# Performance work log

Hardware: AMD Instinct MI355X
Metric: run time of the kernel (lower is better)

## Reference

```python
import jax, jax.numpy as jnp
import numpy as np

E = 1024   # embed_dim
H = 16     # num_heads
HD = E // H
FF = 4096  # hidden_dim
EPS = 1e-5

def _ln(x, g, b):
    mu = jnp.mean(x, axis=-1, keepdims=True)
    var = jnp.mean((x - mu) ** 2, axis=-1, keepdims=True)
    return (x - mu) * jax.lax.rsqrt(var + EPS) * g + b

def setup_inputs() -> dict:
    key = jax.random.key(0)
    ks = jax.random.split(key, 8)
    s = 0.02
    return {
        "x": jax.random.normal(ks[0], (2, 2048, E), dtype=jnp.float32),
        "w_qkv": jax.random.normal(ks[1], (3 * E, E), dtype=jnp.float32) * s,
        "b_qkv": jnp.zeros((3 * E,), dtype=jnp.float32),
        "w_out": jax.random.normal(ks[2], (E, E), dtype=jnp.float32) * s,
        "b_out": jnp.zeros((E,), dtype=jnp.float32),
        "g1": jnp.ones((E,), dtype=jnp.float32),
        "beta1": jnp.zeros((E,), dtype=jnp.float32),
        "g2": jnp.ones((E,), dtype=jnp.float32),
        "beta2": jnp.zeros((E,), dtype=jnp.float32),
        "w1": jax.random.normal(ks[3], (FF, E), dtype=jnp.float32) * s,
        "bf1": jnp.zeros((FF,), dtype=jnp.float32),
        "w2": jax.random.normal(ks[4], (E, FF), dtype=jnp.float32) * s,
        "bf2": jnp.zeros((E,), dtype=jnp.float32),
    }

def reference(x, w_qkv, b_qkv, w_out, b_out, g1, beta1, g2, beta2, w1, bf1, w2, bf2):
    B, S, _ = x.shape
    # qkv projection, then the module's exact reshape: (B,S,H,3*HD) -> (H,B,S,3*HD)
    qkv = (x @ w_qkv.T + b_qkv).reshape(B, S, H, 3 * HD).transpose(2, 0, 1, 3)
    q, k, v = jnp.split(qkv, 3, axis=-1)           # each (H,B,S,HD)
    scores = jnp.einsum('hbqd,hbkd->hbqk', q, k) / (HD ** 0.5)
    attn = jax.nn.softmax(scores, axis=-1)
    ctx = jnp.einsum('hbqk,hbkd->hbqd', attn, v)   # (H,B,S,HD)
    ctx = ctx.transpose(1, 2, 0, 3).reshape(B, S, E)
    attn_out = ctx @ w_out.T + b_out
    x1 = _ln(x + attn_out, g1, beta1)
    # FFN with exact (erf-based) GELU, matching torch nn.GELU default
    h = jax.nn.gelu(x1 @ w1.T + bf1, approximate=False)
    ffn_out = h @ w2.T + bf2
    return _ln(x1 + ffn_out, g2, beta2)
```

## Files before the change

### kernel.cpp

```cpp
#include <hip/hip_runtime.h>
#include <hip/hip_bf16.h>
#include <math.h>

typedef __bf16 bf16x8 __attribute__((ext_vector_type(8)));
typedef __bf16 bf16x4 __attribute__((ext_vector_type(4)));
typedef float  f32x4  __attribute__((ext_vector_type(4)));

#define MFMA16(a, b, c) __builtin_amdgcn_mfma_f32_16x16x32_bf16((a), (b), (c), 0, 0, 0)

__device__ __forceinline__ void gl16(const void* g, void* l) {
  __builtin_amdgcn_global_load_lds(
      (const __attribute__((address_space(1))) unsigned int*)g,
      (__attribute__((address_space(3))) unsigned int*)l, 16, 0, 0);
}

__global__ __launch_bounds__(256) void f32_to_bf16(const float* __restrict__ in,
                                                   __bf16* __restrict__ out, int n) {
  int i = (blockIdx.x * 256 + threadIdx.x) * 4;
  if (i < n) {
    float4 f = *(const float4*)(in + i);
    bf16x4 o = {(__bf16)f.x, (__bf16)f.y, (__bf16)f.z, (__bf16)f.w};
    *(bf16x4*)(out + i) = o;
  }
}

template <int MODE>
__global__ __launch_bounds__(256, 2) void gemm_bt(
    const __bf16* __restrict__ A, const __bf16* __restrict__ Bw,
    const float* __restrict__ bias, const float* __restrict__ resid,
    float* __restrict__ outF, __bf16* __restrict__ outB, int M, int N, int K) {
  __shared__ __bf16 As[128 * 32];
  __shared__ __bf16 Bs[128 * 32];
  const int tid = threadIdx.x;
  const int wave = tid >> 6, lane = tid & 63;
  const int quad = lane >> 4, l16 = lane & 15;
  const int wm = (wave >> 1) * 64, wn = (wave & 1) * 64;
  const long bm = (long)blockIdx.y * 128, bn = (long)blockIdx.x * 128;
  const int r0 = tid >> 2;
  const int c0 = (tid & 3) * 8;
  const __bf16* Ag = A + (bm + r0) * (long)K + c0;
  const __bf16* Bg = Bw + (bn + r0) * (long)K + c0;

  f32x4 acc[4][4] = {};

  for (int k0 = 0; k0 < K; k0 += 32) {
    __syncthreads();
    gl16(Ag + k0, &As[tid * 8]);
    gl16(Ag + 64 * (long)K + k0, &As[2048 + tid * 8]);
    gl16(Bg + k0, &Bs[tid * 8]);
    gl16(Bg + 64 * (long)K + k0, &Bs[2048 + tid * 8]);
    __syncthreads();

    bf16x8 af[4], bfr[4];
#pragma unroll
    for (int mt = 0; mt < 4; mt++)
      af[mt] = *(const bf16x8*)&As[(wm + mt * 16 + l16) * 32 + quad * 8];
#pragma unroll
    for (int nt = 0; nt < 4; nt++)
      bfr[nt] = *(const bf16x8*)&Bs[(wn + nt * 16 + l16) * 32 + quad * 8];
#pragma unroll
    for (int nt = 0; nt < 4; nt++)
#pragma unroll
      for (int mt = 0; mt < 4; mt++)
        acc[mt][nt] = MFMA16(af[mt], bfr[nt], acc[mt][nt]);
  }

#pragma unroll
  for (int mt = 0; mt < 4; mt++) {
#pragma unroll
    for (int nt = 0; nt < 4; nt++) {
#pragma unroll
      for (int r = 0; r < 4; r++) {
        const int row = (int)bm + wm + mt * 16 + quad * 4 + r;
        const int col = (int)bn + wn + nt * 16 + l16;
        float v = acc[mt][nt][r] + bias[col];
        if (MODE == 0) {
          const int b = row >> 11, s = row & 2047;
          const int h = col / 192, rem = col - h * 192;
          const int seg = rem >> 6, d = rem & 63;
          const int hb = h * 2 + b;
          if (seg == 0) {
            v *= 0.180336880111113704f;
            outB[((long)hb * 2048 + s) * 64 + d] = (__bf16)v;
          } else if (seg == 1) {
            outB[4194304L + ((long)hb * 2048 + s) * 64 + d] = (__bf16)v;
          } else {
            const int t = s >> 6, kp = s & 63;
            outB[2 * 4194304L + (((long)hb * 32 + t) * 64 + d) * 64 + kp] = (__bf16)v;
          }
        } else if (MODE == 2) {
          const float g = 0.5f * v * (1.0f + erff(v * 0.70710678118654752f));
          outB[(long)row * N + col] = (__bf16)g;
        } else {
          const long idx = (long)row * N + col;
          outF[idx] = resid[idx] + v;
        }
      }
    }
  }
}

__global__ __launch_bounds__(256, 2) void gemm_bt64(
    const __bf16* __restrict__ A, const __bf16* __restrict__ Bw,
    const float* __restrict__ bias, const float* __restrict__ resid,
    float* __restrict__ outF, int M, int N, int K) {
  __shared__ __bf16 As[64 * 32];
  __shared__ __bf16 Bs[128 * 32];
  const int tid = threadIdx.x;
  const int wave = tid >> 6, lane = tid & 63;
  const int quad = lane >> 4, l16 = lane & 15;
  const int wm = (wave >> 1) * 32, wn = (wave & 1) * 64;
  const long bm = (long)blockIdx.y * 64, bn = (long)blockIdx.x * 128;
  const int r0 = tid >> 2;
  const int c0 = (tid & 3) * 8;
  const __bf16* Ag = A + (bm + r0) * (long)K + c0;
  const __bf16* Bg = Bw + (bn + r0) * (long)K + c0;

  f32x4 acc[2][4] = {};

  for (int k0 = 0; k0 < K; k0 += 32) {
    __syncthreads();
    gl16(Ag + k0, &As[tid * 8]);
    gl16(Bg + k0, &Bs[tid * 8]);
    gl16(Bg + 64 * (long)K + k0, &Bs[2048 + tid * 8]);
    __syncthreads();

    bf16x8 af[2], bfr[4];
#pragma unroll
    for (int mt = 0; mt < 2; mt++)
      af[mt] = *(const bf16x8*)&As[(wm + mt * 16 + l16) * 32 + quad * 8];
#pragma unroll
    for (int nt = 0; nt < 4; nt++)
      bfr[nt] = *(const bf16x8*)&Bs[(wn + nt * 16 + l16) * 32 + quad * 8];
#pragma unroll
    for (int nt = 0; nt < 4; nt++)
#pragma unroll
      for (int mt = 0; mt < 2; mt++)
        acc[mt][nt] = MFMA16(af[mt], bfr[nt], acc[mt][nt]);
  }

#pragma unroll
  for (int mt = 0; mt < 2; mt++)
#pragma unroll
    for (int nt = 0; nt < 4; nt++)
#pragma unroll
      for (int r = 0; r < 4; r++) {
        const int row = (int)bm + wm + mt * 16 + quad * 4 + r;
        const int col = (int)bn + wn + nt * 16 + l16;
        const float v = acc[mt][nt][r] + bias[col];
        const long idx = (long)row * N + col;
        outF[idx] = resid[idx] + v;
      }
}

__global__ __launch_bounds__(256) void flash_attn(const __bf16* __restrict__ Qb,
                                                  const __bf16* __restrict__ Kb,
                                                  const __bf16* __restrict__ Vtb,
                                                  __bf16* __restrict__ ctx) {
  __shared__ __bf16 KsLo[64 * 32], KsHi[64 * 32];
  __shared__ __bf16 VsLo[64 * 32], VsHi[64 * 32];
  __shared__ __bf16 Pb[4][32 * 72];
  const int tid = threadIdx.x;
  const int wave = tid >> 6, lane = tid & 63;
  const int quad = lane >> 4, l16 = lane & 15;
  const int n = blockIdx.x;
  const int hb = n & 31;
  const int qblk = n >> 5;
  const int h = hb >> 1, b = hb & 1;
  const __bf16* Q = Qb + (long)hb * 131072;
  const __bf16* K = Kb + (long)hb * 131072;
  const __bf16* Vt = Vtb + (long)hb * 131072;
  const int qr = qblk * 128 + wave * 32;

  bf16x8 q0[2], q1[2];
#pragma unroll
  for (int rb = 0; rb < 2; rb++) {
    q0[rb] = *(const bf16x8*)&Q[(qr + rb * 16 + l16) * 64 + quad * 8];
    q1[rb] = *(const bf16x8*)&Q[(qr + rb * 16 + l16) * 64 + 32 + quad * 8];
  }

  f32x4 o[2][4] = {};
  f32x4 lp[2] = {};

  const int sr = tid >> 2;
  const int sc = (tid & 3) * 8;

  for (int kt = 0; kt < 2048; kt += 64) {
    __syncthreads();
    gl16(&K[(kt + sr) * 64 + sc], &KsLo[tid * 8]);
    gl16(&K[(kt + sr) * 64 + 32 + sc], &KsHi[tid * 8]);
    const __bf16* Vtile = Vt + (long)(kt >> 6) * 4096;
    gl16(&Vtile[sr * 64 + sc], &VsLo[tid * 8]);
    gl16(&Vtile[sr * 64 + 32 + sc], &VsHi[tid * 8]);
    __syncthreads();

    bf16x8 kf0[4], kf1[4];
#pragma unroll
    for (int nt = 0; nt < 4; nt++) {
      kf0[nt] = *(const bf16x8*)&KsLo[(nt * 16 + l16) * 32 + quad * 8];
      kf1[nt] = *(const bf16x8*)&KsHi[(nt * 16 + l16) * 32 + quad * 8];
    }
    f32x4 s[2][4];
#pragma unroll
    for (int rb = 0; rb < 2; rb++)
#pragma unroll
      for (int nt = 0; nt < 4; nt++) {
        f32x4 z = {};
        z = MFMA16(q0[rb], kf0[nt], z);
        z = MFMA16(q1[rb], kf1[nt], z);
        s[rb][nt] = z;
      }

#pragma unroll
    for (int rb = 0; rb < 2; rb++)
#pragma unroll
      for (int nt = 0; nt < 4; nt++)
#pragma unroll
        for (int r = 0; r < 4; r++) {
          const float p = __builtin_amdgcn_exp2f(s[rb][nt][r]);
          s[rb][nt][r] = p;
          lp[rb][r] += p;
        }

#pragma unroll
    for (int rb = 0; rb < 2; rb++)
#pragma unroll
      for (int nt = 0; nt < 4; nt++)
#pragma unroll
        for (int r = 0; r < 4; r++)
          Pb[wave][(rb * 16 + quad * 4 + r) * 72 + nt * 16 + l16] =
              (__bf16)s[rb][nt][r];

    bf16x8 vf0[4], vf1[4];
#pragma unroll
    for (int nt = 0; nt < 4; nt++) {
      vf0[nt] = *(const bf16x8*)&VsLo[(nt * 16 + l16) * 32 + quad * 8];
      vf1[nt] = *(const bf16x8*)&VsHi[(nt * 16 + l16) * 32 + quad * 8];
    }
#pragma unroll
    for (int rb = 0; rb < 2; rb++) {
      const bf16x8 p0 = *(const bf16x8*)&Pb[wave][(rb * 16 + l16) * 72 + quad * 8];
      const bf16x8 p1 = *(const bf16x8*)&Pb[wave][(rb * 16 + l16) * 72 + 32 + quad * 8];
#pragma unroll
      for (int nt = 0; nt < 4; nt++) {
        o[rb][nt] = MFMA16(p0, vf0[nt], o[rb][nt]);
        o[rb][nt] = MFMA16(p1, vf1[nt], o[rb][nt]);
      }
    }
  }

#pragma unroll
  for (int rb = 0; rb < 2; rb++) {
    float inv[4];
#pragma unroll
    for (int r = 0; r < 4; r++) {
      float l = lp[rb][r];
      l += __shfl_xor(l, 1);
      l += __shfl_xor(l, 2);
      l += __shfl_xor(l, 4);
      l += __shfl_xor(l, 8);
      inv[r] = __builtin_amdgcn_rcpf(l);
    }
#pragma unroll
    for (int nt = 0; nt < 4; nt++)
#pragma unroll
      for (int r = 0; r < 4; r++) {
        const int srow = qr + rb * 16 + quad * 4 + r;
        const float val = o[rb][nt][r] * inv[r];
        const int d = nt * 16 + l16;
        ctx[((long)(b * 2048 + srow)) * 1024 + h * 64 + d] = (__bf16)val;
      }
  }
}

template <int WB>
__global__ __launch_bounds__(256) void layernorm_k(const float* __restrict__ in,
                                                   const float* __restrict__ g,
                                                   const float* __restrict__ be,
                                                   float* __restrict__ outF,
                                                   __bf16* __restrict__ outB) {
  const int tid = threadIdx.x;
  const long row = blockIdx.x;
  const float4 v = ((const float4*)(in + row * 1024))[tid];
  float sum = v.x + v.y + v.z + v.w;
  float sq = v.x * v.x + v.y * v.y + v.z * v.z + v.w * v.w;
#pragma unroll
  for (int m = 32; m >= 1; m >>= 1) {
    sum += __shfl_xor(sum, m);
    sq += __shfl_xor(sq, m);
  }
  __shared__ float red[8];
  const int wave = tid >> 6;
  if ((tid & 63) == 0) {
    red[wave] = sum;
    red[4 + wave] = sq;
  }
  __syncthreads();
  sum = red[0] + red[1] + red[2] + red[3];
  sq = red[4] + red[5] + red[6] + red[7];
  const float mu = sum * (1.f / 1024.f);
  const float var = sq * (1.f / 1024.f) - mu * mu;
  const float rs = rsqrtf(var + 1e-5f);
  const float4 gv = ((const float4*)g)[tid];
  const float4 bv = ((const float4*)be)[tid];
  float4 o;
  o.x = (v.x - mu) * rs * gv.x + bv.x;
  o.y = (v.y - mu) * rs * gv.y + bv.y;
  o.z = (v.z - mu) * rs * gv.z + bv.z;
  o.w = (v.w - mu) * rs * gv.w + bv.w;
  ((float4*)(outF + row * 1024))[tid] = o;
  if (WB) {
    bf16x4 ob = {(__bf16)o.x, (__bf16)o.y, (__bf16)o.z, (__bf16)o.w};
    *(bf16x4*)&outB[row * 1024 + tid * 4] = ob;
  }
}

extern "C" void kernel_launch(void* const* d_in, const int* in_sizes, int n_in,
                              void* d_out, int out_size, void* d_ws, size_t ws_size,
                              hipStream_t stream) {
  const float* x     = (const float*)d_in[0];
  const float* w_qkv = (const float*)d_in[1];
  const float* b_qkv = (const float*)d_in[2];
  const float* w_out = (const float*)d_in[3];
  const float* b_out = (const float*)d_in[4];
  const float* g1    = (const float*)d_in[5];
  const float* be1   = (const float*)d_in[6];
  const float* g2    = (const float*)d_in[7];
  const float* be2   = (const float*)d_in[8];
  const float* w1    = (const float*)d_in[9];
  const float* bf1   = (const float*)d_in[10];
  const float* w2    = (const float*)d_in[11];
  const float* bf2   = (const float*)d_in[12];
  float* out = (float*)d_out;

  char* ws = (char*)d_ws;
  const long MB = 1024L * 1024;
  __bf16* wqkvb = (__bf16*)(ws + 0 * MB);
  __bf16* woutb = (__bf16*)(ws + 6 * MB);
  __bf16* w1b   = (__bf16*)(ws + 8 * MB);
  __bf16* w2b   = (__bf16*)(ws + 16 * MB);
  __bf16* xb    = (__bf16*)(ws + 24 * MB);
  __bf16* qkvb  = (__bf16*)(ws + 32 * MB);
  __bf16* ctxb  = (__bf16*)(ws + 56 * MB);
  float*  res1  = (float*)(ws + 64 * MB);
  __bf16* x1b   = (__bf16*)(ws + 80 * MB);
  __bf16* hb    = (__bf16*)(ws + 32 * MB);
  float*  res2  = (float*)(ws + 0 * MB);

  f32_to_bf16<<<4096, 256, 0, stream>>>(x, xb, 4096 * 1024);
  f32_to_bf16<<<3072, 256, 0, stream>>>(w_qkv, wqkvb, 3072 * 1024);
  f32_to_bf16<<<1024, 256, 0, stream>>>(w_out, woutb, 1024 * 1024);
  f32_to_bf16<<<4096, 256, 0, stream>>>(w1, w1b, 4096 * 1024);
  f32_to_bf16<<<4096, 256, 0, stream>>>(w2, w2b, 1024 * 4096);

  gemm_bt<0><<<dim3(24, 32), 256, 0, stream>>>(xb, wqkvb, b_qkv, nullptr, nullptr,
                                               qkvb, 4096, 3072, 1024);
  flash_attn<<<512, 256, 0, stream>>>(qkvb, qkvb + 4194304,
                                      qkvb + 2 * 4194304, ctxb);
  gemm_bt64<<<dim3(8, 64), 256, 0, stream>>>(ctxb, woutb, b_out, x, res1,
                                             4096, 1024, 1024);
  layernorm_k<1><<<4096, 256, 0, stream>>>(res1, g1, be1, res1, x1b);
  gemm_bt<2><<<dim3(32, 32), 256, 0, stream>>>(x1b, w1b, bf1, nullptr, nullptr, hb,
                                               4096, 4096, 1024);
  gemm_bt64<<<dim3(8, 64), 256, 0, stream>>>(hb, w2b, bf2, res1, res2,
                                             4096, 1024, 4096);
  layernorm_k<0><<<4096, 256, 0, stream>>>(res2, g2, be2, out, nullptr);
}
```

Baseline: 398.2 us.

## Split-K the N=1024 GEMMs and fuse partial reduction into LayerNorm

Replaces the 64-row output-projection and FFN-down GEMMs with a 128x128-tile split-K kernel (4 K-slices). Each slice writes bf16 partial sums into workspace regions that are no longer live. A new reduce_ln kernel sums the partials, adds bias and residual, and applies LayerNorm in one pass. This removes the separate fp32 residual round-trip and gives more parallel blocks for the long-K GEMM. The five weight and input cast launches are also merged into one kernel. Storing partials in bf16 adds extra rounding error, and the scheme depends on carefully aliased workspace buffers.

```diff
diff --git a/kernel.cpp b/kernel.cpp
--- a/kernel.cpp
+++ b/kernel.cpp
@@ -14,21 +14,31 @@
       (__attribute__((address_space(3))) unsigned int*)l, 16, 0, 0);
 }
 
-__global__ __launch_bounds__(256) void f32_to_bf16(const float* __restrict__ in,
-                                                   __bf16* __restrict__ out, int n) {
-  int i = (blockIdx.x * 256 + threadIdx.x) * 4;
-  if (i < n) {
-    float4 f = *(const float4*)(in + i);
-    bf16x4 o = {(__bf16)f.x, (__bf16)f.y, (__bf16)f.z, (__bf16)f.w};
-    *(bf16x4*)(out + i) = o;
-  }
+__global__ __launch_bounds__(256) void cast_all(
+    const float* __restrict__ x, const float* __restrict__ wqkv,
+    const float* __restrict__ wout, const float* __restrict__ w1,
+    const float* __restrict__ w2, __bf16* __restrict__ xb,
+    __bf16* __restrict__ wqkvb, __bf16* __restrict__ woutb,
+    __bf16* __restrict__ w1b, __bf16* __restrict__ w2b) {
+  const long i = ((long)blockIdx.x * 256 + threadIdx.x) * 4;
+  const float* src;
+  __bf16* dst;
+  long off;
+  if (i < 4194304L) { src = x; dst = xb; off = i; }
+  else if (i < 7340032L) { src = wqkv; dst = wqkvb; off = i - 4194304L; }
+  else if (i < 8388608L) { src = wout; dst = woutb; off = i - 7340032L; }
+  else if (i < 12582912L) { src = w1; dst = w1b; off = i - 8388608L; }
+  else { src = w2; dst = w2b; off = i - 12582912L; }
+  const float4 f = *(const float4*)(src + off);
+  bf16x4 o = {(__bf16)f.x, (__bf16)f.y, (__bf16)f.z, (__bf16)f.w};
+  *(bf16x4*)(dst + off) = o;
 }
 
 template <int MODE>
 __global__ __launch_bounds__(256, 2) void gemm_bt(
     const __bf16* __restrict__ A, const __bf16* __restrict__ Bw,
-    const float* __restrict__ bias, const float* __restrict__ resid,
-    float* __restrict__ outF, __bf16* __restrict__ outB, int M, int N, int K) {
+    const float* __restrict__ bias, __bf16* __restrict__ outB,
+    int M, int N, int K) {
   __shared__ __bf16 As[128 * 32];
   __shared__ __bf16 Bs[128 * 32];
   const int tid = threadIdx.x;
@@ -88,46 +98,45 @@
             const int t = s >> 6, kp = s & 63;
             outB[2 * 4194304L + (((long)hb * 32 + t) * 64 + d) * 64 + kp] = (__bf16)v;
           }
-        } else if (MODE == 2) {
+        } else {
           const float g = 0.5f * v * (1.0f + erff(v * 0.70710678118654752f));
           outB[(long)row * N + col] = (__bf16)g;
-        } else {
-          const long idx = (long)row * N + col;
-          outF[idx] = resid[idx] + v;
         }
       }
     }
   }
 }
 
-__global__ __launch_bounds__(256, 2) void gemm_bt64(
+__global__ __launch_bounds__(256, 2) void gemm_split(
     const __bf16* __restrict__ A, const __bf16* __restrict__ Bw,
-    const float* __restrict__ bias, const float* __restrict__ resid,
-    float* __restrict__ outF, int M, int N, int K) {
-  __shared__ __bf16 As[64 * 32];
+    __bf16* __restrict__ Pbase, const long4 offs, int N, int K, int splitK) {
+  __shared__ __bf16 As[128 * 32];
   __shared__ __bf16 Bs[128 * 32];
   const int tid = threadIdx.x;
   const int wave = tid >> 6, lane = tid & 63;
   const int quad = lane >> 4, l16 = lane & 15;
-  const int wm = (wave >> 1) * 32, wn = (wave & 1) * 64;
-  const long bm = (long)blockIdx.y * 64, bn = (long)blockIdx.x * 128;
+  const int wm = (wave >> 1) * 64, wn = (wave & 1) * 64;
+  const long bm = (long)blockIdx.y * 128, bn = (long)blockIdx.x * 128;
+  const int z = blockIdx.z;
+  const long kb = (long)z * splitK;
   const int r0 = tid >> 2;
   const int c0 = (tid & 3) * 8;
-  const __bf16* Ag = A + (bm + r0) * (long)K + c0;
-  const __bf16* Bg = Bw + (bn + r0) * (long)K + c0;
-
-  f32x4 acc[2][4] = {};
-
-  for (int k0 = 0; k0 < K; k0 += 32) {
+  const __bf16* Ag = A + (bm + r0) * (long)K + c0 + kb;
+  const __bf16* Bg = Bw + (bn + r0) * (long)K + c0 + kb;
+
+  f32x4 acc[4][4] = {};
+
+  for (int k0 = 0; k0 < splitK; k0 += 32) {
     __syncthreads();
     gl16(Ag + k0, &As[tid * 8]);
+    gl16(Ag + 64 * (long)K + k0, &As[2048 + tid * 8]);
     gl16(Bg + k0, &Bs[tid * 8]);
     gl16(Bg + 64 * (long)K + k0, &Bs[2048 + tid * 8]);
     __syncthreads();
 
-    bf16x8 af[2], bfr[4];
-#pragma unroll
-    for (int mt = 0; mt < 2; mt++)
+    bf16x8 af[4], bfr[4];
+#pragma unroll
+    for (int mt = 0; mt < 4; mt++)
       af[mt] = *(const bf16x8*)&As[(wm + mt * 16 + l16) * 32 + quad * 8];
 #pragma unroll
     for (int nt = 0; nt < 4; nt++)
@@ -135,22 +144,72 @@
 #pragma unroll
     for (int nt = 0; nt < 4; nt++)
 #pragma unroll
-      for (int mt = 0; mt < 2; mt++)
+      for (int mt = 0; mt < 4; mt++)
         acc[mt][nt] = MFMA16(af[mt], bfr[nt], acc[mt][nt]);
   }
 
-#pragma unroll
-  for (int mt = 0; mt < 2; mt++)
+  const long po = (z == 0) ? offs.x : (z == 1) ? offs.y : (z == 2) ? offs.z : offs.w;
+#pragma unroll
+  for (int mt = 0; mt < 4; mt++)
 #pragma unroll
     for (int nt = 0; nt < 4; nt++)
 #pragma unroll
       for (int r = 0; r < 4; r++) {
         const int row = (int)bm + wm + mt * 16 + quad * 4 + r;
         const int col = (int)bn + wn + nt * 16 + l16;
-        const float v = acc[mt][nt][r] + bias[col];
-        const long idx = (long)row * N + col;
-        outF[idx] = resid[idx] + v;
-      }
+        Pbase[po + (long)row * N + col] = (__bf16)acc[mt][nt][r];
+      }
+}
+
+template <int WB>
+__global__ __launch_bounds__(256) void reduce_ln(
+    const __bf16* __restrict__ Pbase, const long4 offs,
+    const float* __restrict__ resid, const float* __restrict__ bias,
+    const float* __restrict__ g, const float* __restrict__ be,
+    float* __restrict__ outF, __bf16* __restrict__ outB) {
+  const int tid = threadIdx.x;
+  const long row = blockIdx.x;
+  const int c = tid * 4;
+  float4 v = ((const float4*)(resid + row * 1024))[tid];
+  const float4 bb = ((const float4*)bias)[tid];
+  v.x += bb.x; v.y += bb.y; v.z += bb.z; v.w += bb.w;
+  const long lo[4] = {offs.x, offs.y, offs.z, offs.w};
+#pragma unroll
+  for (int s = 0; s < 4; s++) {
+    const bf16x4 p = *(const bf16x4*)&Pbase[lo[s] + row * 1024 + c];
+    v.x += (float)p[0]; v.y += (float)p[1]; v.z += (float)p[2]; v.w += (float)p[3];
+  }
+  float sum = v.x + v.y + v.z + v.w;
+  float sq = v.x * v.x + v.y * v.y + v.z * v.z + v.w * v.w;
+#pragma unroll
+  for (int m = 32; m >= 1; m >>= 1) {
+    sum += __shfl_xor(sum, m);
+    sq += __shfl_xor(sq, m);
+  }
+  __shared__ float red[8];
+  const int wave = tid >> 6;
+  if ((tid & 63) == 0) {
+    red[wave] = sum;
+    red[4 + wave] = sq;
+  }
+  __syncthreads();
+  sum = red[0] + red[1] + red[2] + red[3];
+  sq = red[4] + red[5] + red[6] + red[7];
+  const float mu = sum * (1.f / 1024.f);
+  const float var = sq * (1.f / 1024.f) - mu * mu;
+  const float rs = rsqrtf(var + 1e-5f);
+  const float4 gv = ((const float4*)g)[tid];
+  const float4 bv = ((const float4*)be)[tid];
+  float4 o;
+  o.x = (v.x - mu) * rs * gv.x + bv.x;
+  o.y = (v.y - mu) * rs * gv.y + bv.y;
+  o.z = (v.z - mu) * rs * gv.z + bv.z;
+  o.w = (v.w - mu) * rs * gv.w + bv.w;
+  ((float4*)(outF + row * 1024))[tid] = o;
+  if (WB) {
+    bf16x4 ob = {(__bf16)o.x, (__bf16)o.y, (__bf16)o.z, (__bf16)o.w};
+    *(bf16x4*)&outB[row * 1024 + c] = ob;
+  }
 }
 
 __global__ __launch_bounds__(256) void flash_attn(const __bf16* __restrict__ Qb,
@@ -273,48 +332,6 @@
   }
 }
 
-template <int WB>
-__global__ __launch_bounds__(256) void layernorm_k(const float* __restrict__ in,
-                                                   const float* __restrict__ g,
-                                                   const float* __restrict__ be,
-                                                   float* __restrict__ outF,
-                                                   __bf16* __restrict__ outB) {
-  const int tid = threadIdx.x;
-  const long row = blockIdx.x;
-  const float4 v = ((const float4*)(in + row * 1024))[tid];
-  float sum = v.x + v.y + v.z + v.w;
-  float sq = v.x * v.x + v.y * v.y + v.z * v.z + v.w * v.w;
-#pragma unroll
-  for (int m = 32; m >= 1; m >>= 1) {
-    sum += __shfl_xor(sum, m);
-    sq += __shfl_xor(sq, m);
-  }
-  __shared__ float red[8];
-  const int wave = tid >> 6;
-  if ((tid & 63) == 0) {
-    red[wave] = sum;
-    red[4 + wave] = sq;
-  }
-  __syncthreads();
-  sum = red[0] + red[1] + red[2] + red[3];
-  sq = red[4] + red[5] + red[6] + red[7];
-  const float mu = sum * (1.f / 1024.f);
-  const float var = sq * (1.f / 1024.f) - mu * mu;
-  const float rs = rsqrtf(var + 1e-5f);
-  const float4 gv = ((const float4*)g)[tid];
-  const float4 bv = ((const float4*)be)[tid];
-  float4 o;
-  o.x = (v.x - mu) * rs * gv.x + bv.x;
-  o.y = (v.y - mu) * rs * gv.y + bv.y;
-  o.z = (v.z - mu) * rs * gv.z + bv.z;
-  o.w = (v.w - mu) * rs * gv.w + bv.w;
-  ((float4*)(outF + row * 1024))[tid] = o;
-  if (WB) {
-    bf16x4 ob = {(__bf16)o.x, (__bf16)o.y, (__bf16)o.z, (__bf16)o.w};
-    *(bf16x4*)&outB[row * 1024 + tid * 4] = ob;
-  }
-}
-
 extern "C" void kernel_launch(void* const* d_in, const int* in_sizes, int n_in,
                               void* d_out, int out_size, void* d_ws, size_t ws_size,
                               hipStream_t stream) {
@@ -335,6 +352,7 @@
 
   char* ws = (char*)d_ws;
   const long MB = 1024L * 1024;
+  __bf16* wsb   = (__bf16*)ws;
   __bf16* wqkvb = (__bf16*)(ws + 0 * MB);
   __bf16* woutb = (__bf16*)(ws + 6 * MB);
   __bf16* w1b   = (__bf16*)(ws + 8 * MB);
@@ -344,25 +362,26 @@
   __bf16* ctxb  = (__bf16*)(ws + 56 * MB);
   float*  res1  = (float*)(ws + 64 * MB);
   __bf16* x1b   = (__bf16*)(ws + 80 * MB);
-  __bf16* hb    = (__bf16*)(ws + 32 * MB);
-  float*  res2  = (float*)(ws + 0 * MB);
-
-  f32_to_bf16<<<4096, 256, 0, stream>>>(x, xb, 4096 * 1024);
-  f32_to_bf16<<<3072, 256, 0, stream>>>(w_qkv, wqkvb, 3072 * 1024);
-  f32_to_bf16<<<1024, 256, 0, stream>>>(w_out, woutb, 1024 * 1024);
-  f32_to_bf16<<<4096, 256, 0, stream>>>(w1, w1b, 4096 * 1024);
-  f32_to_bf16<<<4096, 256, 0, stream>>>(w2, w2b, 1024 * 4096);
-
-  gemm_bt<0><<<dim3(24, 32), 256, 0, stream>>>(xb, wqkvb, b_qkv, nullptr, nullptr,
-                                               qkvb, 4096, 3072, 1024);
+  __bf16* hb    = (__bf16*)(ws + 24 * MB);
+
+  const long4 offs_op = {24 * 524288L, 32 * 524288L, 40 * 524288L, 48 * 524288L};
+  const long4 offs_f2 = {0 * 524288L, 8 * 524288L, 56 * 524288L, 80 * 524288L};
+
+  cast_all<<<16384, 256, 0, stream>>>(x, w_qkv, w_out, w1, w2,
+                                      xb, wqkvb, woutb, w1b, w2b);
+
+  gemm_bt<0><<<dim3(24, 32), 256, 0, stream>>>(xb, wqkvb, b_qkv, qkvb,
+                                               4096, 3072, 1024);
   flash_attn<<<512, 256, 0, stream>>>(qkvb, qkvb + 4194304,
                                       qkvb + 2 * 4194304, ctxb);
-  gemm_bt64<<<dim3(8, 64), 256, 0, stream>>>(ctxb, woutb, b_out, x, res1,
-                                             4096, 1024, 1024);
-  layernorm_k<1><<<4096, 256, 0, stream>>>(res1, g1, be1, res1, x1b);
-  gemm_bt<2><<<dim3(32, 32), 256, 0, stream>>>(x1b, w1b, bf1, nullptr, nullptr, hb,
+  gemm_split<<<dim3(8, 32, 4), 256, 0, stream>>>(ctxb, woutb, wsb, offs_op,
+                                                 1024, 1024, 256);
+  reduce_ln<1><<<4096, 256, 0, stream>>>(wsb, offs_op, x, b_out, g1, be1,
+                                         res1, x1b);
+  gemm_bt<2><<<dim3(32, 32), 256, 0, stream>>>(x1b, w1b, bf1, hb,
                                                4096, 4096, 1024);
-  gemm_bt64<<<dim3(8, 64), 256, 0, stream>>>(hb, w2b, bf2, res1, res2,
-                                             4096, 1024, 4096);
-  layernorm_k<0><<<4096, 256, 0, stream>>>(res2, g2, be2, out, nullptr);
-}
+  gemm_split<<<dim3(8, 32, 4), 256, 0, stream>>>(hb, w2b, wsb, offs_f2,
+                                                 1024, 4096, 1024);
+  reduce_ln<0><<<4096, 256, 0, stream>>>(wsb, offs_f2, res1, bf2, g2, be2,
+                                         out, nullptr);
+}
```

Result: faster. 369.5 us (-7.2%).
